# Performance work log

Hardware: AMD Instinct MI355X
Metric: run time of the kernel (lower is better)

The kernel has to match this reference:

```python
import jax, jax.numpy as jnp
import numpy as np

B, T, D_MODEL = 2, 2048, 2048
NH, NKV, DH = 16, 4, 128
N_REP = NH // NKV
NV = 256  # n_vision_tokens
THETA = 10000.0
NEG = -1e9


def setup_inputs() -> dict:
    key = jax.random.key(0)
    ks = jax.random.split(key, 5)
    x = jax.random.normal(ks[0], (B, T, D_MODEL), jnp.float32)
    # rope_freqs = exp(i * t * theta^{-2j/D}) represented as cos/sin, shape [T, DH//2]
    inv = 1.0 / (THETA ** (np.arange(0, DH, 2, dtype=np.float64) / DH))
    ang = np.outer(np.arange(T, dtype=np.float64), inv)
    cos = jnp.asarray(np.cos(ang), jnp.float32)
    sin = jnp.asarray(np.sin(ang), jnp.float32)
    sc = 0.02
    wq = jax.random.normal(ks[1], (D_MODEL, NH * DH), jnp.float32) * sc
    wk = jax.random.normal(ks[2], (D_MODEL, NKV * DH), jnp.float32) * sc
    wv = jax.random.normal(ks[3], (D_MODEL, NKV * DH), jnp.float32) * sc
    wo = jax.random.normal(ks[4], (NH * DH, D_MODEL), jnp.float32) * sc
    return {"x": x, "cos": cos, "sin": sin, "wq": wq, "wk": wk, "wv": wv,
            "wo": wo, "n_vision_tokens": NV}


def _rope(t, cos, sin):
    # t: [B,H,L,D]; pairs (even=real, odd=imag); cos/sin: [L, D//2]
    a = t[..., 0::2]
    b = t[..., 1::2]
    c = cos[None, None]
    s = sin[None, None]
    ra = a * c - b * s
    rb = a * s + b * c
    return jnp.stack([ra, rb], axis=-1).reshape(t.shape)


def reference(x, cos, sin, wq, wk, wv, wo, n_vision_tokens):
    Bx, Tx, _ = x.shape
    nv = int(n_vision_tokens)
    tl = Tx - nv  # text length

    q = (x @ wq).reshape(Bx, Tx, NH, DH).transpose(0, 2, 1, 3)   # [B,NH,T,DH]
    k = (x @ wk).reshape(Bx, Tx, NKV, DH).transpose(0, 2, 1, 3)  # [B,NKV,T,DH]
    v = (x @ wv).reshape(Bx, Tx, NKV, DH).transpose(0, 2, 1, 3)

    # RoPE only on the text portion (vision tokens keep raw q/k)
    c, s = cos[:tl], sin[:tl]
    q = jnp.concatenate([q[:, :, :nv], _rope(q[:, :, nv:], c, s)], axis=2)
    k = jnp.concatenate([k[:, :, :nv], _rope(k[:, :, nv:], c, s)], axis=2)

    new_kv_cache = (k, v)

    # GQA: repeat_interleave KV heads
    k = jnp.repeat(k, N_REP, axis=1)
    v = jnp.repeat(v, N_REP, axis=1)

    attn = jnp.einsum('bhqd,bhkd->bhqk', q, k) / jnp.sqrt(jnp.float32(DH))

    # hybrid mask: vision rows/cols fully visible; text-text strictly causal
    text_mask = jnp.triu(jnp.ones((tl, tl), bool), k=1)
    mask = jnp.zeros((Tx, Tx), bool).at[nv:, nv:].set(text_mask)
    attn = jnp.where(mask[None, None], NEG, attn)

    attn = jax.nn.softmax(attn, axis=-1)
    out = jnp.einsum('bhqk,bhkd->bhqd', attn, v)
    out = out.transpose(0, 2, 1, 3).reshape(Bx, Tx, NH * DH) @ wo
    return out, new_kv_cache
```

## Files before the change

### kernel.cpp

```cpp
#include <hip/hip_runtime.h>
#include <hip/hip_bf16.h>

#define BB 2
#define TT 2048
#define DMODEL 2048
#define NH 16
#define NKV 4
#define DH 128
#define NV 256
#define TL (TT - NV)
#define NQKV 3072

typedef __bf16  bf16x8  __attribute__((ext_vector_type(8)));
typedef float   float4v __attribute__((ext_vector_type(4)));
typedef short   short8  __attribute__((ext_vector_type(8)));
typedef unsigned short ushort;

__device__ __forceinline__ float bf2f(ushort u) {
    union { float f; unsigned i; } c; c.i = ((unsigned)u) << 16; return c.f;
}
__device__ __forceinline__ ushort f2bf(float f) {
    union { float f; unsigned i; } c; c.f = f;
    unsigned r = c.i + 0x7fff + ((c.i >> 16) & 1);
    return (ushort)(r >> 16);
}
__device__ __forceinline__ unsigned cvtpk(float a, float b) {
    unsigned r;
    asm("v_cvt_pk_bf16_f32 %0, %1, %2" : "=v"(r) : "v"(a), "v"(b));
    return r;
}

#define GLDS16(g, l) __builtin_amdgcn_global_load_lds( \
    (__attribute__((address_space(1))) void*)(g), \
    (__attribute__((address_space(3))) void*)(l), 16, 0, 0)

__global__ __launch_bounds__(256) void convert_x(
    const float* __restrict__ x, ushort* __restrict__ xbf)
{
    size_t i = ((size_t)blockIdx.x * 256 + threadIdx.x) * 8;
    float4v f0 = *(const float4v*)&x[i];
    float4v f1 = *(const float4v*)&x[i + 4];
    short8 h;
    h[0] = (short)f2bf(f0[0]); h[1] = (short)f2bf(f0[1]);
    h[2] = (short)f2bf(f0[2]); h[3] = (short)f2bf(f0[3]);
    h[4] = (short)f2bf(f1[0]); h[5] = (short)f2bf(f1[1]);
    h[6] = (short)f2bf(f1[2]); h[7] = (short)f2bf(f1[3]);
    *(short8*)&xbf[i] = h;
}

__global__ __launch_bounds__(256) void wtrans(
    const float* __restrict__ w, ushort* __restrict__ wT, int K, int N)
{
    __shared__ ushort st[64][72];
    int n0 = blockIdx.x * 64, k0 = blockIdx.y * 64;
    int r  = threadIdx.x >> 2;
    int c0 = (threadIdx.x & 3) * 16;
    #pragma unroll
    for (int j = 0; j < 16; j += 4) {
        float4v f = *(const float4v*)&w[(size_t)(k0 + r) * N + n0 + c0 + j];
        st[c0 + j + 0][r] = f2bf(f[0]);
        st[c0 + j + 1][r] = f2bf(f[1]);
        st[c0 + j + 2][r] = f2bf(f[2]);
        st[c0 + j + 3][r] = f2bf(f[3]);
    }
    __syncthreads();
    ushort* dst = &wT[(size_t)(n0 + r) * K + k0];
    *(short8*)&dst[c0]     = *(short8*)&st[r][c0];
    *(short8*)&dst[c0 + 8] = *(short8*)&st[r][c0 + 8];
}

__global__ __launch_bounds__(256) void wtrans_wo(
    const float* __restrict__ w, ushort* __restrict__ qkv)
{
    __shared__ ushort st[64][72];
    int n0 = blockIdx.x * 64, k0 = blockIdx.y * 64;
    int r  = threadIdx.x >> 2;
    int c0 = (threadIdx.x & 3) * 16;
    #pragma unroll
    for (int j = 0; j < 16; j += 4) {
        float4v f = *(const float4v*)&w[(size_t)(k0 + r) * DMODEL + n0 + c0 + j];
        st[c0 + j + 0][r] = f2bf(f[0]);
        st[c0 + j + 1][r] = f2bf(f[1]);
        st[c0 + j + 2][r] = f2bf(f[2]);
        st[c0 + j + 3][r] = f2bf(f[3]);
    }
    __syncthreads();
    ushort* dst = qkv + ((size_t)(2 * (n0 + r) + (k0 >> 10))) * NQKV + 2048 + (k0 & 1023);
    *(short8*)&dst[c0]     = *(short8*)&st[r][c0];
    *(short8*)&dst[c0 + 8] = *(short8*)&st[r][c0 + 8];
}

__global__ __launch_bounds__(256) void vtrans(
    const ushort* __restrict__ qkv, ushort* __restrict__ vbfT)
{
    __shared__ ushort st[64][72];
    int t0 = blockIdx.x * 64, d0 = blockIdx.y * 64;
    int bk = blockIdx.z;
    int b = bk >> 2, kh = bk & 3;
    int r  = threadIdx.x >> 2;
    int c0 = (threadIdx.x & 3) * 16;
    const ushort* src = qkv + ((size_t)(b * TT + t0 + r)) * NQKV + 2560 + kh * DH + d0;
    short8 a0 = *(const short8*)&src[c0];
    short8 a1 = *(const short8*)&src[c0 + 8];
    #pragma unroll
    for (int j = 0; j < 8; j++) {
        st[c0 + j][r]     = (ushort)a0[j];
        st[c0 + 8 + j][r] = (ushort)a1[j];
    }
    __syncthreads();
    ushort* dst = vbfT + ((size_t)(bk * DH + d0 + r)) * TT + t0;
    *(short8*)&dst[c0]     = *(short8*)&st[r][c0];
    *(short8*)&dst[c0 + 8] = *(short8*)&st[r][c0 + 8];
}

__global__ __launch_bounds__(256) void gemm_lds(
    const ushort* __restrict__ A, int lda,
    const ushort* __restrict__ BT,
    ushort* __restrict__ C, int ldc, int K)
{
    __shared__ ushort As[128 * 32];
    __shared__ ushort Bs[128 * 32];

    int tid = threadIdx.x;
    int wave = tid >> 6, lane = tid & 63, quad = lane >> 4, l16 = lane & 15;
    int m0 = blockIdx.y * 128, n0 = blockIdx.x * 128;
    int wr = (wave >> 1) * 64, wc = (wave & 1) * 64;

    int srow = tid >> 2, scol = (tid & 3) * 8;
    const ushort* ag = A  + (size_t)(m0 + srow) * lda + scol;
    const ushort* bg = BT + (size_t)(n0 + srow) * K   + scol;
    ushort* la0 = As + (wave * 16) * 32;
    ushort* la1 = As + (64 + wave * 16) * 32;
    ushort* lb0 = Bs + (wave * 16) * 32;
    ushort* lb1 = Bs + (64 + wave * 16) * 32;

    float4v acc[4][4];
    for (int i = 0; i < 4; i++)
        for (int j = 0; j < 4; j++)
            acc[i][j] = (float4v){0.f, 0.f, 0.f, 0.f};

    for (int k0 = 0; k0 < K; k0 += 32) {
        GLDS16(ag + k0,                     la0);
        GLDS16(ag + (size_t)64 * lda + k0,  la1);
        GLDS16(bg + k0,                     lb0);
        GLDS16(bg + (size_t)64 * K + k0,    lb1);
        __syncthreads();

        bf16x8 af[4], bfr[4];
        #pragma unroll
        for (int i = 0; i < 4; i++) af[i] = *(const bf16x8*)&As[(wr + i * 16 + l16) * 32 + quad * 8];
        #pragma unroll
        for (int j = 0; j < 4; j++) bfr[j] = *(const bf16x8*)&Bs[(wc + j * 16 + l16) * 32 + quad * 8];
        #pragma unroll
        for (int i = 0; i < 4; i++)
            #pragma unroll
            for (int j = 0; j < 4; j++)
                acc[i][j] = __builtin_amdgcn_mfma_f32_16x16x32_bf16(af[i], bfr[j], acc[i][j], 0, 0, 0);
        __syncthreads();
    }

    #pragma unroll
    for (int i = 0; i < 4; i++)
        #pragma unroll
        for (int j = 0; j < 4; j++)
            #pragma unroll
            for (int r = 0; r < 4; r++) {
                int row = m0 + wr + i * 16 + quad * 4 + r;
                int col = n0 + wc + j * 16 + l16;
                C[(size_t)row * ldc + col] = f2bf(acc[i][j][r]);
            }
}

__global__ __launch_bounds__(256) void gemm_out(
    const ushort* __restrict__ A,
    const ushort* __restrict__ Bc,
    float* __restrict__ C)
{
    __shared__ ushort As[128 * 32];
    __shared__ ushort Bs[128 * 32];

    int tid = threadIdx.x;
    int wave = tid >> 6, lane = tid & 63, quad = lane >> 4, l16 = lane & 15;
    int m0 = blockIdx.y * 128, n0 = blockIdx.x * 128;
    int wr = (wave >> 1) * 64, wc = (wave & 1) * 64;

    int srow = tid >> 2, scol = (tid & 3) * 8;
    const ushort* ag = A  + (size_t)(m0 + srow) * NQKV + scol;
    const ushort* bg = Bc + (size_t)(n0 + srow) * 6144 + scol;
    ushort* la0 = As + (wave * 16) * 32;
    ushort* la1 = As + (64 + wave * 16) * 32;
    ushort* lb0 = Bs + (wave * 16) * 32;
    ushort* lb1 = Bs + (64 + wave * 16) * 32;

    float4v acc[4][4];
    for (int i = 0; i < 4; i++)
        for (int j = 0; j < 4; j++)
            acc[i][j] = (float4v){0.f, 0.f, 0.f, 0.f};

    for (int k0 = 0; k0 < 2048; k0 += 32) {
        int koff = ((k0 >> 10) * NQKV) + (k0 & 1023);
        GLDS16(ag + k0,                       la0);
        GLDS16(ag + (size_t)64 * NQKV + k0,   la1);
        GLDS16(bg + koff,                     lb0);
        GLDS16(bg + (size_t)64 * 6144 + koff, lb1);
        __syncthreads();

        bf16x8 af[4], bfr[4];
        #pragma unroll
        for (int i = 0; i < 4; i++) af[i] = *(const bf16x8*)&As[(wr + i * 16 + l16) * 32 + quad * 8];
        #pragma unroll
        for (int j = 0; j < 4; j++) bfr[j] = *(const bf16x8*)&Bs[(wc + j * 16 + l16) * 32 + quad * 8];
        #pragma unroll
        for (int i = 0; i < 4; i++)
            #pragma unroll
            for (int j = 0; j < 4; j++)
                acc[i][j] = __builtin_amdgcn_mfma_f32_16x16x32_bf16(af[i], bfr[j], acc[i][j], 0, 0, 0);
        __syncthreads();
    }

    #pragma unroll
    for (int i = 0; i < 4; i++)
        #pragma unroll
        for (int j = 0; j < 4; j++)
            #pragma unroll
            for (int r = 0; r < 4; r++) {
                int row = m0 + wr + i * 16 + quad * 4 + r;
                int col = n0 + wc + j * 16 + l16;
                C[(size_t)row * DMODEL + col] = acc[i][j][r];
            }
}

__global__ __launch_bounds__(256) void rope_q(
    ushort* __restrict__ qkv, const float* __restrict__ cosp, const float* __restrict__ sinp)
{
    int idx = blockIdx.x * 256 + threadIdx.x;
    int b = blockIdx.y;
    int i  = idx & 63;
    int h  = (idx >> 6) & 15;
    int tr = idx >> 10;
    int t  = NV + tr;
    size_t off = ((size_t)(b * TT + t)) * NQKV + h * DH + 2 * i;
    unsigned pk = *(const unsigned*)&qkv[off];
    float a  = bf2f((ushort)(pk & 0xffff));
    float bb = bf2f((ushort)(pk >> 16));
    float c  = cosp[tr * 64 + i];
    float s  = sinp[tr * 64 + i];
    *(unsigned*)&qkv[off] = (unsigned)f2bf(a * c - bb * s) | ((unsigned)f2bf(a * s + bb * c) << 16);
}

__global__ __launch_bounds__(256) void ropek_cache(
    const ushort* __restrict__ qkv,
    const float* __restrict__ cosp, const float* __restrict__ sinp,
    float* __restrict__ kout, float* __restrict__ vout, ushort* __restrict__ kbf)
{
    int idx = blockIdx.x * 256 + threadIdx.x;
    int i  = idx & 63;
    int kh = (idx >> 6) & 3;
    int t  = (idx >> 8) & 2047;
    int b  = idx >> 19;
    size_t row = ((size_t)(b * TT + t)) * NQKV;
    size_t dst = ((size_t)((b * NKV + kh) * TT + t)) * DH + 2 * i;
    unsigned pk = *(const unsigned*)&qkv[row + 2048 + kh * DH + 2 * i];
    float ka = bf2f((ushort)(pk & 0xffff));
    float kb = bf2f((ushort)(pk >> 16));
    if (t >= NV) {
        int pos = t - NV;
        float c = cosp[pos * 64 + i];
        float s = sinp[pos * 64 + i];
        float ra = ka * c - kb * s;
        float rb = ka * s + kb * c;
        ka = ra; kb = rb;
    }
    kout[dst]     = ka;
    kout[dst + 1] = kb;
    *(unsigned*)&kbf[dst] = (unsigned)f2bf(ka) | ((unsigned)f2bf(kb) << 16);
    unsigned pv = *(const unsigned*)&qkv[row + 2560 + kh * DH + 2 * i];
    vout[dst]     = bf2f((ushort)(pv & 0xffff));
    vout[dst + 1] = bf2f((ushort)(pv >> 16));
}

__global__ __launch_bounds__(256, 2) void attn_kernel(
    ushort* qkv,
    const ushort* __restrict__ kbf, const ushort* __restrict__ vbfT)
{
    __shared__ ushort shm[32768];

    int tid = threadIdx.x;
    int wave = tid >> 6, lane = tid & 63, quad = lane >> 4, l16 = lane & 15;
    int qx = blockIdx.x;
    int qt = (qx < 4) ? qx : (35 - qx);
    int hy = blockIdx.y, b = blockIdx.z;
    int h0 = hy * 2;
    int kh = hy >> 1;
    int q0 = qt * 64;

    int srow = tid >> 2, scol = (tid & 3) * 8;

    ushort* qbase0 = qkv + ((size_t)(b * TT) + q0) * NQKV + h0 * DH;
    ushort* qbase1 = qbase0 + DH;
    #pragma unroll
    for (int dk = 0; dk < 4; dk++) {
        GLDS16(qbase0 + (size_t)srow * NQKV + dk * 32 + scol, shm + dk * 2048 + wave * 512);
        GLDS16(qbase1 + (size_t)srow * NQKV + dk * 32 + scol, shm + 16384 + dk * 2048 + wave * 512);
    }
    __syncthreads();
    bf16x8 qf0[4], qf1[4];
    #pragma unroll
    for (int dk = 0; dk < 4; dk++) {
        qf0[dk] = *(const bf16x8*)&shm[dk * 2048 + (wave * 16 + l16) * 32 + quad * 8];
        qf1[dk] = *(const bf16x8*)&shm[16384 + dk * 2048 + (wave * 16 + l16) * 32 + quad * 8];
    }
    __syncthreads();

    float4v O0[8], O1[8];
    #pragma unroll
    for (int i = 0; i < 8; i++) {
        O0[i] = (float4v){0.f, 0.f, 0.f, 0.f};
        O1[i] = (float4v){0.f, 0.f, 0.f, 0.f};
    }
    float m0r = -1e30f, l0r = 0.f;
    float m1r = -1e30f, l1r = 0.f;

    int nkt = (q0 < NV) ? (TT / 64) : (qt + 1);
    const float scale = 0.08838834764831845f;
    int qg = q0 + wave * 16 + l16;

    const ushort* kb2 = kbf  + ((size_t)(b * NKV + kh)) * TT * DH;
    const ushort* vb2 = vbfT + ((size_t)(b * NKV + kh)) * DH * TT;

    int sl0 = ((lane & 16) << 1) + l16;
    int sl1 = sl0 + 16;
    bool hi = lane >= 32;

    auto stage = [&](int buf, int kt) {
        ushort* Kb = shm + buf * 16384;
        ushort* Vb = Kb + 8192;
        int k0 = kt * 64;
        #pragma unroll
        for (int dk = 0; dk < 4; dk++)
            GLDS16(kb2 + (size_t)(k0 + srow) * DH + dk * 32 + scol, Kb + dk * 2048 + wave * 512);
        #pragma unroll
        for (int kk = 0; kk < 2; kk++)
            #pragma unroll
            for (int p = 0; p < 2; p++)
                GLDS16(vb2 + (size_t)(p * 64 + srow) * TT + k0 + kk * 32 + scol,
                       Vb + kk * 4096 + (p * 64 + wave * 16) * 32);
    };

    stage(0, 0);

    for (int kt = 0; kt < nkt; kt++) {
        int cur = kt & 1;
        __syncthreads();
        if (kt + 1 < nkt)
            stage(cur ^ 1, kt + 1);

        const ushort* Kc = shm + cur * 16384;
        const ushort* Vc = Kc + 8192;
        int k0 = kt * 64;

        float4v s0[4], s1[4];
        __builtin_amdgcn_s_setprio(1);
        #pragma unroll
        for (int t2i = 0; t2i < 4; t2i++) {
            float4v a0 = (float4v){0.f, 0.f, 0.f, 0.f};
            float4v a1 = (float4v){0.f, 0.f, 0.f, 0.f};
            #pragma unroll
            for (int dk = 0; dk < 4; dk++) {
                bf16x8 af = *(const bf16x8*)&Kc[dk * 2048 + (t2i * 16 + l16) * 32 + quad * 8];
                a0 = __builtin_amdgcn_mfma_f32_16x16x32_bf16(af, qf0[dk], a0, 0, 0, 0);
                a1 = __builtin_amdgcn_mfma_f32_16x16x32_bf16(af, qf1[dk], a1, 0, 0, 0);
            }
            s0[t2i] = a0; s1[t2i] = a1;
        }
        __builtin_amdgcn_s_setprio(0);

        bool diag = (q0 >= NV) && (kt == qt);
        #pragma unroll
        for (int t2i = 0; t2i < 4; t2i++)
            #pragma unroll
            for (int i = 0; i < 4; i++) {
                bool msk = diag && (k0 + t2i * 16 + quad * 4 + i > qg);
                float v0 = s0[t2i][i] * scale; if (msk) v0 = -1e9f; s0[t2i][i] = v0;
                float v1 = s1[t2i][i] * scale; if (msk) v1 = -1e9f; s1[t2i][i] = v1;
            }

        float mx0 = -1e30f, mx1 = -1e30f;
        #pragma unroll
        for (int t2i = 0; t2i < 4; t2i++)
            #pragma unroll
            for (int i = 0; i < 4; i++) {
                mx0 = fmaxf(mx0, s0[t2i][i]);
                mx1 = fmaxf(mx1, s1[t2i][i]);
            }
        mx0 = fmaxf(mx0, __shfl_xor(mx0, 16, 64));
        mx0 = fmaxf(mx0, __shfl_xor(mx0, 32, 64));
        mx1 = fmaxf(mx1, __shfl_xor(mx1, 16, 64));
        mx1 = fmaxf(mx1, __shfl_xor(mx1, 32, 64));

        bool skip0 = __all(mx0 <= m0r + 8.f);
        bool skip1 = __all(mx1 <= m1r + 8.f);
        float mn0 = fmaxf(m0r, mx0), mn1 = fmaxf(m1r, mx1);
        float mref0 = skip0 ? m0r : mn0;
        float mref1 = skip1 ? m1r : mn1;

        float ss0 = 0.f, ss1 = 0.f;
        #pragma unroll
        for (int t2i = 0; t2i < 4; t2i++)
            #pragma unroll
            for (int i = 0; i < 4; i++) {
                float p0 = __expf(s0[t2i][i] - mref0); s0[t2i][i] = p0; ss0 += p0;
                float p1 = __expf(s1[t2i][i] - mref1); s1[t2i][i] = p1; ss1 += p1;
            }
        ss0 += __shfl_xor(ss0, 16, 64); ss0 += __shfl_xor(ss0, 32, 64);
        ss1 += __shfl_xor(ss1, 16, 64); ss1 += __shfl_xor(ss1, 32, 64);

        if (!skip0) {
            float al0 = __expf(m0r - mn0);
            #pragma unroll
            for (int dt = 0; dt < 8; dt++)
                #pragma unroll
                for (int i = 0; i < 4; i++) O0[dt][i] *= al0;
            l0r *= al0;
            m0r = mn0;
        }
        l0r += ss0;
        if (!skip1) {
            float al1 = __expf(m1r - mn1);
            #pragma unroll
            for (int dt = 0; dt < 8; dt++)
                #pragma unroll
                for (int i = 0; i < 4; i++) O1[dt][i] *= al1;
            l1r *= al1;
            m1r = mn1;
        }
        l1r += ss1;

        unsigned p01a[4], p23a[4], p01b[4], p23b[4];
        #pragma unroll
        for (int t2i = 0; t2i < 4; t2i++) {
            p01a[t2i] = cvtpk(s0[t2i][0], s0[t2i][1]);
            p23a[t2i] = cvtpk(s0[t2i][2], s0[t2i][3]);
            p01b[t2i] = cvtpk(s1[t2i][0], s1[t2i][1]);
            p23b[t2i] = cvtpk(s1[t2i][2], s1[t2i][3]);
        }

        #pragma unroll
        for (int kk = 0; kk < 2; kk++) {
            int ta = 2 * kk, tb = 2 * kk + 1;
            union { unsigned u[4]; bf16x8 v; } pf0, pf1;
            {
                unsigned A0 = __shfl(p01a[ta], sl0, 64), B0 = __shfl(p01a[tb], sl0, 64);
                unsigned A1 = __shfl(p23a[ta], sl0, 64), B1 = __shfl(p23a[tb], sl0, 64);
                unsigned A2 = __shfl(p01a[ta], sl1, 64), B2 = __shfl(p01a[tb], sl1, 64);
                unsigned A3 = __shfl(p23a[ta], sl1, 64), B3 = __shfl(p23a[tb], sl1, 64);
                pf0.u[0] = hi ? B0 : A0;
                pf0.u[1] = hi ? B1 : A1;
                pf0.u[2] = hi ? B2 : A2;
                pf0.u[3] = hi ? B3 : A3;
            }
            {
                unsigned A0 = __shfl(p01b[ta], sl0, 64), B0 = __shfl(p01b[tb], sl0, 64);
                unsigned A1 = __shfl(p23b[ta], sl0, 64), B1 = __shfl(p23b[tb], sl0, 64);
                unsigned A2 = __shfl(p01b[ta], sl1, 64), B2 = __shfl(p01b[tb], sl1, 64);
                unsigned A3 = __shfl(p23b[ta], sl1, 64), B3 = __shfl(p23b[tb], sl1, 64);
                pf1.u[0] = hi ? B0 : A0;
                pf1.u[1] = hi ? B1 : A1;
                pf1.u[2] = hi ? B2 : A2;
                pf1.u[3] = hi ? B3 : A3;
            }
            __builtin_amdgcn_s_setprio(1);
            #pragma unroll
            for (int dt = 0; dt < 8; dt++) {
                bf16x8 vf = *(const bf16x8*)&Vc[kk * 4096 + (dt * 16 + l16) * 32 + quad * 8];
                O0[dt] = __builtin_amdgcn_mfma_f32_16x16x32_bf16(vf, pf0.v, O0[dt], 0, 0, 0);
                O1[dt] = __builtin_amdgcn_mfma_f32_16x16x32_bf16(vf, pf1.v, O1[dt], 0, 0, 0);
            }
            __builtin_amdgcn_s_setprio(0);
        }
    }

    float rinv0 = 1.f / l0r, rinv1 = 1.f / l1r;
    size_t orow = (size_t)(wave * 16 + l16) * NQKV;
    #pragma unroll
    for (int dt = 0; dt < 8; dt++)
        #pragma unroll
        for (int i = 0; i < 4; i += 2) {
            unsigned pk0 = cvtpk(O0[dt][i] * rinv0, O0[dt][i + 1] * rinv0);
            unsigned pk1 = cvtpk(O1[dt][i] * rinv1, O1[dt][i + 1] * rinv1);
            *(unsigned*)&qbase0[orow + dt * 16 + quad * 4 + i] = pk0;
            *(unsigned*)&qbase1[orow + dt * 16 + quad * 4 + i] = pk1;
        }
}

extern "C" void kernel_launch(void* const* d_in, const int* in_sizes, int n_in,
                              void* d_out, int out_size, void* d_ws, size_t ws_size,
                              hipStream_t stream) {
    const float* x    = (const float*)d_in[0];
    const float* cosp = (const float*)d_in[1];
    const float* sinp = (const float*)d_in[2];
    const float* wq   = (const float*)d_in[3];
    const float* wk   = (const float*)d_in[4];
    const float* wv   = (const float*)d_in[5];
    const float* wo   = (const float*)d_in[6];

    float* out  = (float*)d_out;
    float* kout = out + (size_t)BB * TT * DMODEL;
    float* vout = kout + (size_t)BB * NKV * TT * DH;

    ushort* sc    = (ushort*)d_out;
    ushort* wqkvT = sc;
    ushort* xbf   = sc + (size_t)NQKV * DMODEL;
    ushort* kbf   = sc + (size_t)NQKV * DMODEL;
    ushort* vbfT  = kbf + (size_t)BB * NKV * TT * DH;

    ushort* qkv = (ushort*)d_ws;

    const int M = BB * TT;

    convert_x<<<dim3((size_t)M * DMODEL / 2048), 256, 0, stream>>>(x, xbf);
    wtrans<<<dim3(DMODEL / 64, DMODEL / 64), 256, 0, stream>>>(wq, wqkvT, DMODEL, DMODEL);
    wtrans<<<dim3((NKV * DH) / 64, DMODEL / 64), 256, 0, stream>>>(wk, wqkvT + (size_t)2048 * DMODEL, DMODEL, NKV * DH);
    wtrans<<<dim3((NKV * DH) / 64, DMODEL / 64), 256, 0, stream>>>(wv, wqkvT + (size_t)2560 * DMODEL, DMODEL, NKV * DH);

    gemm_lds<<<dim3(NQKV / 128, M / 128), 256, 0, stream>>>(
        xbf, DMODEL, wqkvT, qkv, NQKV, DMODEL);

    rope_q<<<dim3(TL * NH * 64 / 256, BB), 256, 0, stream>>>(qkv, cosp, sinp);
    ropek_cache<<<dim3((BB * TT * NKV * 64) / 256), 256, 0, stream>>>(qkv, cosp, sinp, kout, vout, kbf);
    vtrans<<<dim3(TT / 64, DH / 64, BB * NKV), 256, 0, stream>>>(qkv, vbfT);

    wtrans_wo<<<dim3(DMODEL / 64, DMODEL / 64), 256, 0, stream>>>(wo, qkv);

    attn_kernel<<<dim3(TT / 64, NH / 2, BB), 256, 0, stream>>>(qkv, kbf, vbfT);

    gemm_out<<<dim3(DMODEL / 128, M / 128), 256, 0, stream>>>(qkv, qkv + 2048, out);
}
```

Baseline: 373.8 us.

## Double-buffer GEMM LDS loads, swizzle tiles, fuse post-processing kernels, fold softmax scale

The two GEMMs now double-buffer their LDS tiles, so the next K-slice is loaded while MFMAs run on the current one. This also removes one barrier per iteration. Workgroup IDs are swizzled in groups of 8 to improve cache locality. The q/k/v weight transposes become one launch, and the RoPE-q, RoPE-k/cache and V-transpose kernels are merged into one postproc launch, cutting launch overhead. The attention kernel reorders its grid so heads sharing a query tile run together, and folds the softmax scale into an FMA inside exp with a scaled lazy-rescale threshold, at the cost of more code complexity.

```diff
diff --git a/kernel.cpp b/kernel.cpp
--- a/kernel.cpp
+++ b/kernel.cpp
@@ -48,23 +48,28 @@
     *(short8*)&xbf[i] = h;
 }
 
-__global__ __launch_bounds__(256) void wtrans(
-    const float* __restrict__ w, ushort* __restrict__ wT, int K, int N)
+__global__ __launch_bounds__(256) void wtrans_all(
+    const float* __restrict__ wq, const float* __restrict__ wk,
+    const float* __restrict__ wv, ushort* __restrict__ wT)
 {
     __shared__ ushort st[64][72];
     int n0 = blockIdx.x * 64, k0 = blockIdx.y * 64;
+    const float* w; int N, nn;
+    if (n0 < 2048)      { w = wq; N = 2048; nn = n0; }
+    else if (n0 < 2560) { w = wk; N = 512;  nn = n0 - 2048; }
+    else                { w = wv; N = 512;  nn = n0 - 2560; }
     int r  = threadIdx.x >> 2;
     int c0 = (threadIdx.x & 3) * 16;
     #pragma unroll
     for (int j = 0; j < 16; j += 4) {
-        float4v f = *(const float4v*)&w[(size_t)(k0 + r) * N + n0 + c0 + j];
+        float4v f = *(const float4v*)&w[(size_t)(k0 + r) * N + nn + c0 + j];
         st[c0 + j + 0][r] = f2bf(f[0]);
         st[c0 + j + 1][r] = f2bf(f[1]);
         st[c0 + j + 2][r] = f2bf(f[2]);
         st[c0 + j + 3][r] = f2bf(f[3]);
     }
     __syncthreads();
-    ushort* dst = &wT[(size_t)(n0 + r) * K + k0];
+    ushort* dst = &wT[(size_t)(n0 + r) * DMODEL + k0];
     *(short8*)&dst[c0]     = *(short8*)&st[r][c0];
     *(short8*)&dst[c0 + 8] = *(short8*)&st[r][c0 + 8];
 }
@@ -90,27 +95,80 @@
     *(short8*)&dst[c0 + 8] = *(short8*)&st[r][c0 + 8];
 }
 
-__global__ __launch_bounds__(256) void vtrans(
-    const ushort* __restrict__ qkv, ushort* __restrict__ vbfT)
+#define RQ_BLOCKS 14336
+#define RK_BLOCKS 4096
+__global__ __launch_bounds__(256) void postproc(
+    ushort* __restrict__ qkv,
+    const float* __restrict__ cosp, const float* __restrict__ sinp,
+    float* __restrict__ kout, float* __restrict__ vout,
+    ushort* __restrict__ kbf, ushort* __restrict__ vbfT)
 {
     __shared__ ushort st[64][72];
-    int t0 = blockIdx.x * 64, d0 = blockIdx.y * 64;
-    int bk = blockIdx.z;
-    int b = bk >> 2, kh = bk & 3;
-    int r  = threadIdx.x >> 2;
-    int c0 = (threadIdx.x & 3) * 16;
-    const ushort* src = qkv + ((size_t)(b * TT + t0 + r)) * NQKV + 2560 + kh * DH + d0;
-    short8 a0 = *(const short8*)&src[c0];
-    short8 a1 = *(const short8*)&src[c0 + 8];
-    #pragma unroll
-    for (int j = 0; j < 8; j++) {
-        st[c0 + j][r]     = (ushort)a0[j];
-        st[c0 + 8 + j][r] = (ushort)a1[j];
-    }
-    __syncthreads();
-    ushort* dst = vbfT + ((size_t)(bk * DH + d0 + r)) * TT + t0;
-    *(short8*)&dst[c0]     = *(short8*)&st[r][c0];
-    *(short8*)&dst[c0 + 8] = *(short8*)&st[r][c0 + 8];
+    int bid = blockIdx.x;
+    if (bid < RQ_BLOCKS) {
+        int b   = bid / (RQ_BLOCKS / 2);
+        int idx = (bid % (RQ_BLOCKS / 2)) * 256 + threadIdx.x;
+        int i  = idx & 63;
+        int h  = (idx >> 6) & 15;
+        int tr = idx >> 10;
+        int t  = NV + tr;
+        size_t off = ((size_t)(b * TT + t)) * NQKV + h * DH + 2 * i;
+        unsigned pk = *(const unsigned*)&qkv[off];
+        float a  = bf2f((ushort)(pk & 0xffff));
+        float bb = bf2f((ushort)(pk >> 16));
+        float c  = cosp[tr * 64 + i];
+        float s  = sinp[tr * 64 + i];
+        *(unsigned*)&qkv[off] = cvtpk(a * c - bb * s, a * s + bb * c);
+        return;
+    }
+    bid -= RQ_BLOCKS;
+    if (bid < RK_BLOCKS) {
+        int idx = bid * 256 + threadIdx.x;
+        int i  = idx & 63;
+        int kh = (idx >> 6) & 3;
+        int t  = (idx >> 8) & 2047;
+        int b  = idx >> 19;
+        size_t row = ((size_t)(b * TT + t)) * NQKV;
+        size_t dst = ((size_t)((b * NKV + kh) * TT + t)) * DH + 2 * i;
+        unsigned pk = *(const unsigned*)&qkv[row + 2048 + kh * DH + 2 * i];
+        float ka = bf2f((ushort)(pk & 0xffff));
+        float kb = bf2f((ushort)(pk >> 16));
+        if (t >= NV) {
+            int pos = t - NV;
+            float c = cosp[pos * 64 + i];
+            float s = sinp[pos * 64 + i];
+            float ra = ka * c - kb * s;
+            float rb = ka * s + kb * c;
+            ka = ra; kb = rb;
+        }
+        kout[dst]     = ka;
+        kout[dst + 1] = kb;
+        *(unsigned*)&kbf[dst] = cvtpk(ka, kb);
+        unsigned pv = *(const unsigned*)&qkv[row + 2560 + kh * DH + 2 * i];
+        vout[dst]     = bf2f((ushort)(pv & 0xffff));
+        vout[dst + 1] = bf2f((ushort)(pv >> 16));
+        return;
+    }
+    bid -= RK_BLOCKS;
+    {
+        int bx = bid & 31, by = (bid >> 5) & 1, bk = bid >> 6;
+        int t0 = bx * 64, d0 = by * 64;
+        int b = bk >> 2, kh = bk & 3;
+        int r  = threadIdx.x >> 2;
+        int c0 = (threadIdx.x & 3) * 16;
+        const ushort* src = qkv + ((size_t)(b * TT + t0 + r)) * NQKV + 2560 + kh * DH + d0;
+        short8 a0 = *(const short8*)&src[c0];
+        short8 a1 = *(const short8*)&src[c0 + 8];
+        #pragma unroll
+        for (int j = 0; j < 8; j++) {
+            st[c0 + j][r]     = (ushort)a0[j];
+            st[c0 + 8 + j][r] = (ushort)a1[j];
+        }
+        __syncthreads();
+        ushort* dst = vbfT + ((size_t)(bk * DH + d0 + r)) * TT + t0;
+        *(short8*)&dst[c0]     = *(short8*)&st[r][c0];
+        *(short8*)&dst[c0 + 8] = *(short8*)&st[r][c0 + 8];
+    }
 }
 
 __global__ __launch_bounds__(256) void gemm_lds(
@@ -118,45 +176,55 @@
     const ushort* __restrict__ BT,
     ushort* __restrict__ C, int ldc, int K)
 {
-    __shared__ ushort As[128 * 32];
-    __shared__ ushort Bs[128 * 32];
+    __shared__ ushort As[2][128 * 32];
+    __shared__ ushort Bs[2][128 * 32];
 
     int tid = threadIdx.x;
     int wave = tid >> 6, lane = tid & 63, quad = lane >> 4, l16 = lane & 15;
-    int m0 = blockIdx.y * 128, n0 = blockIdx.x * 128;
+
+    int nwg = gridDim.x * gridDim.y;
+    int bid = blockIdx.x + gridDim.x * blockIdx.y;
+    int cpx = nwg >> 3;
+    int swz = (bid & 7) * cpx + (bid >> 3);
+    int bx = swz % gridDim.x, by = swz / gridDim.x;
+    int m0 = by * 128, n0 = bx * 128;
     int wr = (wave >> 1) * 64, wc = (wave & 1) * 64;
 
     int srow = tid >> 2, scol = (tid & 3) * 8;
     const ushort* ag = A  + (size_t)(m0 + srow) * lda + scol;
     const ushort* bg = BT + (size_t)(n0 + srow) * K   + scol;
-    ushort* la0 = As + (wave * 16) * 32;
-    ushort* la1 = As + (64 + wave * 16) * 32;
-    ushort* lb0 = Bs + (wave * 16) * 32;
-    ushort* lb1 = Bs + (64 + wave * 16) * 32;
+    int lo0 = (wave * 16) * 32;
+    int lo1 = (64 + wave * 16) * 32;
 
     float4v acc[4][4];
     for (int i = 0; i < 4; i++)
         for (int j = 0; j < 4; j++)
             acc[i][j] = (float4v){0.f, 0.f, 0.f, 0.f};
 
-    for (int k0 = 0; k0 < K; k0 += 32) {
-        GLDS16(ag + k0,                     la0);
-        GLDS16(ag + (size_t)64 * lda + k0,  la1);
-        GLDS16(bg + k0,                     lb0);
-        GLDS16(bg + (size_t)64 * K + k0,    lb1);
+    auto stage = [&](int buf, int k0) {
+        GLDS16(ag + k0,                    As[buf] + lo0);
+        GLDS16(ag + (size_t)64 * lda + k0, As[buf] + lo1);
+        GLDS16(bg + k0,                    Bs[buf] + lo0);
+        GLDS16(bg + (size_t)64 * K + k0,   Bs[buf] + lo1);
+    };
+
+    stage(0, 0);
+    int it = 0;
+    for (int k0 = 0; k0 < K; k0 += 32, ++it) {
+        int cur = it & 1;
         __syncthreads();
+        if (k0 + 32 < K) stage(cur ^ 1, k0 + 32);
 
         bf16x8 af[4], bfr[4];
         #pragma unroll
-        for (int i = 0; i < 4; i++) af[i] = *(const bf16x8*)&As[(wr + i * 16 + l16) * 32 + quad * 8];
-        #pragma unroll
-        for (int j = 0; j < 4; j++) bfr[j] = *(const bf16x8*)&Bs[(wc + j * 16 + l16) * 32 + quad * 8];
+        for (int i = 0; i < 4; i++) af[i] = *(const bf16x8*)&As[cur][(wr + i * 16 + l16) * 32 + quad * 8];
+        #pragma unroll
+        for (int j = 0; j < 4; j++) bfr[j] = *(const bf16x8*)&Bs[cur][(wc + j * 16 + l16) * 32 + quad * 8];
         #pragma unroll
         for (int i = 0; i < 4; i++)
             #pragma unroll
             for (int j = 0; j < 4; j++)
                 acc[i][j] = __builtin_amdgcn_mfma_f32_16x16x32_bf16(af[i], bfr[j], acc[i][j], 0, 0, 0);
-        __syncthreads();
     }
 
     #pragma unroll
@@ -176,46 +244,56 @@
     const ushort* __restrict__ Bc,
     float* __restrict__ C)
 {
-    __shared__ ushort As[128 * 32];
-    __shared__ ushort Bs[128 * 32];
+    __shared__ ushort As[2][128 * 32];
+    __shared__ ushort Bs[2][128 * 32];
 
     int tid = threadIdx.x;
     int wave = tid >> 6, lane = tid & 63, quad = lane >> 4, l16 = lane & 15;
-    int m0 = blockIdx.y * 128, n0 = blockIdx.x * 128;
+
+    int nwg = gridDim.x * gridDim.y;
+    int bid = blockIdx.x + gridDim.x * blockIdx.y;
+    int cpx = nwg >> 3;
+    int swz = (bid & 7) * cpx + (bid >> 3);
+    int bx = swz % gridDim.x, by = swz / gridDim.x;
+    int m0 = by * 128, n0 = bx * 128;
     int wr = (wave >> 1) * 64, wc = (wave & 1) * 64;
 
     int srow = tid >> 2, scol = (tid & 3) * 8;
     const ushort* ag = A  + (size_t)(m0 + srow) * NQKV + scol;
     const ushort* bg = Bc + (size_t)(n0 + srow) * 6144 + scol;
-    ushort* la0 = As + (wave * 16) * 32;
-    ushort* la1 = As + (64 + wave * 16) * 32;
-    ushort* lb0 = Bs + (wave * 16) * 32;
-    ushort* lb1 = Bs + (64 + wave * 16) * 32;
+    int lo0 = (wave * 16) * 32;
+    int lo1 = (64 + wave * 16) * 32;
 
     float4v acc[4][4];
     for (int i = 0; i < 4; i++)
         for (int j = 0; j < 4; j++)
             acc[i][j] = (float4v){0.f, 0.f, 0.f, 0.f};
 
-    for (int k0 = 0; k0 < 2048; k0 += 32) {
+    auto stage = [&](int buf, int k0) {
         int koff = ((k0 >> 10) * NQKV) + (k0 & 1023);
-        GLDS16(ag + k0,                       la0);
-        GLDS16(ag + (size_t)64 * NQKV + k0,   la1);
-        GLDS16(bg + koff,                     lb0);
-        GLDS16(bg + (size_t)64 * 6144 + koff, lb1);
+        GLDS16(ag + k0,                       As[buf] + lo0);
+        GLDS16(ag + (size_t)64 * NQKV + k0,   As[buf] + lo1);
+        GLDS16(bg + koff,                     Bs[buf] + lo0);
+        GLDS16(bg + (size_t)64 * 6144 + koff, Bs[buf] + lo1);
+    };
+
+    stage(0, 0);
+    int it = 0;
+    for (int k0 = 0; k0 < 2048; k0 += 32, ++it) {
+        int cur = it & 1;
         __syncthreads();
+        if (k0 + 32 < 2048) stage(cur ^ 1, k0 + 32);
 
         bf16x8 af[4], bfr[4];
         #pragma unroll
-        for (int i = 0; i < 4; i++) af[i] = *(const bf16x8*)&As[(wr + i * 16 + l16) * 32 + quad * 8];
-        #pragma unroll
-        for (int j = 0; j < 4; j++) bfr[j] = *(const bf16x8*)&Bs[(wc + j * 16 + l16) * 32 + quad * 8];
+        for (int i = 0; i < 4; i++) af[i] = *(const bf16x8*)&As[cur][(wr + i * 16 + l16) * 32 + quad * 8];
+        #pragma unroll
+        for (int j = 0; j < 4; j++) bfr[j] = *(const bf16x8*)&Bs[cur][(wc + j * 16 + l16) * 32 + quad * 8];
         #pragma unroll
         for (int i = 0; i < 4; i++)
             #pragma unroll
             for (int j = 0; j < 4; j++)
                 acc[i][j] = __builtin_amdgcn_mfma_f32_16x16x32_bf16(af[i], bfr[j], acc[i][j], 0, 0, 0);
-        __syncthreads();
     }
 
     #pragma unroll
@@ -230,55 +308,6 @@
             }
 }
 
-__global__ __launch_bounds__(256) void rope_q(
-    ushort* __restrict__ qkv, const float* __restrict__ cosp, const float* __restrict__ sinp)
-{
-    int idx = blockIdx.x * 256 + threadIdx.x;
-    int b = blockIdx.y;
-    int i  = idx & 63;
-    int h  = (idx >> 6) & 15;
-    int tr = idx >> 10;
-    int t  = NV + tr;
-    size_t off = ((size_t)(b * TT + t)) * NQKV + h * DH + 2 * i;
-    unsigned pk = *(const unsigned*)&qkv[off];
-    float a  = bf2f((ushort)(pk & 0xffff));
-    float bb = bf2f((ushort)(pk >> 16));
-    float c  = cosp[tr * 64 + i];
-    float s  = sinp[tr * 64 + i];
-    *(unsigned*)&qkv[off] = (unsigned)f2bf(a * c - bb * s) | ((unsigned)f2bf(a * s + bb * c) << 16);
-}
-
-__global__ __launch_bounds__(256) void ropek_cache(
-    const ushort* __restrict__ qkv,
-    const float* __restrict__ cosp, const float* __restrict__ sinp,
-    float* __restrict__ kout, float* __restrict__ vout, ushort* __restrict__ kbf)
-{
-    int idx = blockIdx.x * 256 + threadIdx.x;
-    int i  = idx & 63;
-    int kh = (idx >> 6) & 3;
-    int t  = (idx >> 8) & 2047;
-    int b  = idx >> 19;
-    size_t row = ((size_t)(b * TT + t)) * NQKV;
-    size_t dst = ((size_t)((b * NKV + kh) * TT + t)) * DH + 2 * i;
-    unsigned pk = *(const unsigned*)&qkv[row + 2048 + kh * DH + 2 * i];
-    float ka = bf2f((ushort)(pk & 0xffff));
-    float kb = bf2f((ushort)(pk >> 16));
-    if (t >= NV) {
-        int pos = t - NV;
-        float c = cosp[pos * 64 + i];
-        float s = sinp[pos * 64 + i];
-        float ra = ka * c - kb * s;
-        float rb = ka * s + kb * c;
-        ka = ra; kb = rb;
-    }
-    kout[dst]     = ka;
-    kout[dst + 1] = kb;
-    *(unsigned*)&kbf[dst] = (unsigned)f2bf(ka) | ((unsigned)f2bf(kb) << 16);
-    unsigned pv = *(const unsigned*)&qkv[row + 2560 + kh * DH + 2 * i];
-    vout[dst]     = bf2f((ushort)(pv & 0xffff));
-    vout[dst + 1] = bf2f((ushort)(pv >> 16));
-}
-
 __global__ __launch_bounds__(256, 2) void attn_kernel(
     ushort* qkv,
     const ushort* __restrict__ kbf, const ushort* __restrict__ vbfT)
@@ -287,9 +316,10 @@
 
     int tid = threadIdx.x;
     int wave = tid >> 6, lane = tid & 63, quad = lane >> 4, l16 = lane & 15;
-    int qx = blockIdx.x;
+    int hy = blockIdx.x;
+    int qx = blockIdx.y;
     int qt = (qx < 4) ? qx : (35 - qx);
-    int hy = blockIdx.y, b = blockIdx.z;
+    int b  = blockIdx.z;
     int h0 = hy * 2;
     int kh = hy >> 1;
     int q0 = qt * 64;
@@ -323,6 +353,7 @@
 
     int nkt = (q0 < NV) ? (TT / 64) : (qt + 1);
     const float scale = 0.08838834764831845f;
+    const float THRR  = 90.50966799f;
     int qg = q0 + wave * 16 + l16;
 
     const ushort* kb2 = kbf  + ((size_t)(b * NKV + kh)) * TT * DH;
@@ -375,15 +406,16 @@
         }
         __builtin_amdgcn_s_setprio(0);
 
-        bool diag = (q0 >= NV) && (kt == qt);
-        #pragma unroll
-        for (int t2i = 0; t2i < 4; t2i++)
-            #pragma unroll
-            for (int i = 0; i < 4; i++) {
-                bool msk = diag && (k0 + t2i * 16 + quad * 4 + i > qg);
-                float v0 = s0[t2i][i] * scale; if (msk) v0 = -1e9f; s0[t2i][i] = v0;
-                float v1 = s1[t2i][i] * scale; if (msk) v1 = -1e9f; s1[t2i][i] = v1;
-            }
+        if ((q0 >= NV) && (kt == qt)) {
+            #pragma unroll
+            for (int t2i = 0; t2i < 4; t2i++)
+                #pragma unroll
+                for (int i = 0; i < 4; i++)
+                    if (k0 + t2i * 16 + quad * 4 + i > qg) {
+                        s0[t2i][i] = -1e9f;
+                        s1[t2i][i] = -1e9f;
+                    }
+        }
 
         float mx0 = -1e30f, mx1 = -1e30f;
         #pragma unroll
@@ -398,25 +430,27 @@
         mx1 = fmaxf(mx1, __shfl_xor(mx1, 16, 64));
         mx1 = fmaxf(mx1, __shfl_xor(mx1, 32, 64));
 
-        bool skip0 = __all(mx0 <= m0r + 8.f);
-        bool skip1 = __all(mx1 <= m1r + 8.f);
+        bool skip0 = __all(mx0 <= m0r + THRR);
+        bool skip1 = __all(mx1 <= m1r + THRR);
         float mn0 = fmaxf(m0r, mx0), mn1 = fmaxf(m1r, mx1);
         float mref0 = skip0 ? m0r : mn0;
         float mref1 = skip1 ? m1r : mn1;
+        float nb0 = -mref0 * scale;
+        float nb1 = -mref1 * scale;
 
         float ss0 = 0.f, ss1 = 0.f;
         #pragma unroll
         for (int t2i = 0; t2i < 4; t2i++)
             #pragma unroll
             for (int i = 0; i < 4; i++) {
-                float p0 = __expf(s0[t2i][i] - mref0); s0[t2i][i] = p0; ss0 += p0;
-                float p1 = __expf(s1[t2i][i] - mref1); s1[t2i][i] = p1; ss1 += p1;
+                float p0 = __expf(__builtin_fmaf(s0[t2i][i], scale, nb0)); s0[t2i][i] = p0; ss0 += p0;
+                float p1 = __expf(__builtin_fmaf(s1[t2i][i], scale, nb1)); s1[t2i][i] = p1; ss1 += p1;
             }
         ss0 += __shfl_xor(ss0, 16, 64); ss0 += __shfl_xor(ss0, 32, 64);
         ss1 += __shfl_xor(ss1, 16, 64); ss1 += __shfl_xor(ss1, 32, 64);
 
         if (!skip0) {
-            float al0 = __expf(m0r - mn0);
+            float al0 = __expf((m0r - mn0) * scale);
             #pragma unroll
             for (int dt = 0; dt < 8; dt++)
                 #pragma unroll
@@ -426,7 +460,7 @@
         }
         l0r += ss0;
         if (!skip1) {
-            float al1 = __expf(m1r - mn1);
+            float al1 = __expf((m1r - mn1) * scale);
             #pragma unroll
             for (int dt = 0; dt < 8; dt++)
                 #pragma unroll
@@ -519,20 +553,17 @@
     const int M = BB * TT;
 
     convert_x<<<dim3((size_t)M * DMODEL / 2048), 256, 0, stream>>>(x, xbf);
-    wtrans<<<dim3(DMODEL / 64, DMODEL / 64), 256, 0, stream>>>(wq, wqkvT, DMODEL, DMODEL);
-    wtrans<<<dim3((NKV * DH) / 64, DMODEL / 64), 256, 0, stream>>>(wk, wqkvT + (size_t)2048 * DMODEL, DMODEL, NKV * DH);
-    wtrans<<<dim3((NKV * DH) / 64, DMODEL / 64), 256, 0, stream>>>(wv, wqkvT + (size_t)2560 * DMODEL, DMODEL, NKV * DH);
+    wtrans_all<<<dim3(NQKV / 64, DMODEL / 64), 256, 0, stream>>>(wq, wk, wv, wqkvT);
 
     gemm_lds<<<dim3(NQKV / 128, M / 128), 256, 0, stream>>>(
         xbf, DMODEL, wqkvT, qkv, NQKV, DMODEL);
 
-    rope_q<<<dim3(TL * NH * 64 / 256, BB), 256, 0, stream>>>(qkv, cosp, sinp);
-    ropek_cache<<<dim3((BB * TT * NKV * 64) / 256), 256, 0, stream>>>(qkv, cosp, sinp, kout, vout, kbf);
-    vtrans<<<dim3(TT / 64, DH / 64, BB * NKV), 256, 0, stream>>>(qkv, vbfT);
+    postproc<<<dim3(RQ_BLOCKS + RK_BLOCKS + 512), 256, 0, stream>>>(
+        qkv, cosp, sinp, kout, vout, kbf, vbfT);
 
     wtrans_wo<<<dim3(DMODEL / 64, DMODEL / 64), 256, 0, stream>>>(wo, qkv);
 
-    attn_kernel<<<dim3(TT / 64, NH / 2, BB), 256, 0, stream>>>(qkv, kbf, vbfT);
+    attn_kernel<<<dim3(NH / 2, TT / 64, BB), 256, 0, stream>>>(qkv, kbf, vbfT);
 
     gemm_out<<<dim3(DMODEL / 128, M / 128), 256, 0, stream>>>(qkv, qkv + 2048, out);
 }
```

Result: faster. 355.3 us (-4.9%).
